# Kernel tuning notes

Hardware: AMD Instinct MI355X
Metric: run time of the kernel (lower is better)

Reference implementation:

```python
import jax, jax.numpy as jnp
import numpy as np

EXTENT = 1.0  # kernel-point influence radius (init kwarg 'extent')
B, N, M, H, K, F, C = 4, 16384, 16384, 32, 15, 64, 64


def setup_inputs() -> dict:
    key = jax.random.key(0)
    ks = jax.random.split(key, 6)
    points = jax.random.uniform(ks[0], (B, N, 3), dtype=jnp.float32)
    features = jax.random.normal(ks[1], (B, N, F), dtype=jnp.float32)
    output_points = jax.random.uniform(ks[2], (B, M, 3), dtype=jnp.float32)
    neighbor_indices = jax.random.randint(ks[3], (B, M, H), 0, N)
    # kernel point dispositions inside a ball of radius 1.5*extent (load_kernels stand-in)
    k_points = jax.random.uniform(ks[4], (K, 3), minval=-1.0, maxval=1.0, dtype=jnp.float32) * (1.5 * EXTENT) / jnp.sqrt(3.0)
    k_values = jax.random.normal(ks[5], (K, F, C), dtype=jnp.float32) * 0.05
    return {
        'points': points, 'features': features, 'output_points': output_points,
        'k_points': k_points, 'k_values': k_values, 'neighbor_indices': neighbor_indices,
    }


def reference(points, features, output_points, k_points, k_values, neighbor_indices):
    b, m, h = neighbor_indices.shape
    idx = neighbor_indices.reshape(b, m * h, 1)
    # batched gather (tf.gather batch_dims=1)
    neigh_pts = jnp.take_along_axis(points, idx, axis=1).reshape(b, m, h, 3)
    neigh_feat = jnp.take_along_axis(features, idx, axis=1).reshape(b, m, h, -1)
    # relative coords to each output point, then to each kernel point
    rel = neigh_pts - output_points[:, :, None, :]                # [B,M,H,3]
    diff = rel[:, :, :, None, :] - k_points                       # [B,M,H,K,3]
    sq_d = jnp.sum(diff * diff, axis=-1)                          # [B,M,H,K]
    # linear influence
    w = jnp.maximum(1.0 - jnp.sqrt(sq_d) / EXTENT, 0.0)           # [B,M,H,K]
    # weight neighbor features per kernel point, then apply per-kernel linear map, sum over K
    wf = jnp.einsum('bmhk,bmhf->bmkf', w, neigh_feat)             # [B,M,K,F]
    out = jnp.einsum('bmkf,kfc->bmc', wf, k_values)               # [B,M,C]
    return out
```

## Files before the change

kernel.cpp:

```cpp
#include <hip/hip_runtime.h>

#define BATCH 4
#define NPTS 16384
#define MPTS 16384
#define NH 32
#define NK 15
#define NF 64
#define NC 64
#define MT 16

typedef short short8 __attribute__((ext_vector_type(8)));
typedef float floatx4 __attribute__((ext_vector_type(4)));

__device__ __forceinline__ unsigned short f2bf(float x) {
    unsigned int u = __builtin_bit_cast(unsigned int, x);
    u = u + 0x7FFFu + ((u >> 16) & 1u);
    return (unsigned short)(u >> 16);
}

__device__ __forceinline__ unsigned pack_trunc(float lo, float hi) {
    return __builtin_amdgcn_perm(__builtin_bit_cast(unsigned, hi),
                                 __builtin_bit_cast(unsigned, lo), 0x07060302u);
}

__global__ void feat_cvt_kernel(const float* __restrict__ src, unsigned short* __restrict__ dst) {
    const int gid = blockIdx.x * 256 + threadIdx.x;
    const size_t base = (size_t)gid * 8;
    float4 a = *(const float4*)(src + base);
    float4 b = *(const float4*)(src + base + 4);
    uint4 o;
    o.x = (unsigned)f2bf(a.x) | ((unsigned)f2bf(a.y) << 16);
    o.y = (unsigned)f2bf(a.z) | ((unsigned)f2bf(a.w) << 16);
    o.z = (unsigned)f2bf(b.x) | ((unsigned)f2bf(b.y) << 16);
    o.w = (unsigned)f2bf(b.z) | ((unsigned)f2bf(b.w) << 16);
    *(uint4*)(dst + base) = o;
}

__global__ void vprep_kernel(const float* __restrict__ kv, unsigned short* __restrict__ vp) {
    const int gid = blockIdx.x * 256 + threadIdx.x;
    const int lane = gid & 63;
    const int ct   = (gid >> 6) & 3;
    const int kk   = gid >> 8;
    const int c    = ct * 16 + (lane & 15);
    const int kap0 = kk * 32 + (lane >> 4) * 8;
    unsigned int o[4];
    #pragma unroll
    for (int jj = 0; jj < 4; jj++) {
        unsigned short lo, hi;
        {
            const int kap = kap0 + jj * 2;
            const int f = kap >> 4, k = kap & 15;
            lo = (k < NK) ? f2bf(kv[((size_t)(k * NF + f)) * NC + c]) : (unsigned short)0;
        }
        {
            const int kap = kap0 + jj * 2 + 1;
            const int f = kap >> 4, k = kap & 15;
            hi = (k < NK) ? f2bf(kv[((size_t)(k * NF + f)) * NC + c]) : (unsigned short)0;
        }
        o[jj] = (unsigned)lo | ((unsigned)hi << 16);
    }
    *(uint4*)(vp + (size_t)gid * 8) = make_uint4(o[0], o[1], o[2], o[3]);
}

__global__ __launch_bounds__(256, 3) void kpconv_kernel(
    const float* __restrict__ points,
    const unsigned short* __restrict__ featbf,
    const float* __restrict__ outpts,
    const float* __restrict__ kpts,
    const unsigned short* __restrict__ vp,
    const int*   __restrict__ nbr,
    float* __restrict__ out)
{
    __shared__ unsigned short awf[32 * 512];
    __shared__ unsigned short feat_s[4 * 1288];
    __shared__ float4 rel_s[4 * 32];
    __shared__ int   idx_s[512];
    __shared__ float opt_s[48];
    __shared__ float kp_s[48];

    const int tid   = threadIdx.x;
    const int batch = blockIdx.x >> 10;
    const int m0    = (blockIdx.x & 1023) << 4;

    if (tid < 48) kp_s[tid] = (tid < 45) ? kpts[tid] : 1e9f;
    if (tid >= 64 && tid < 112)
        opt_s[tid - 64] = outpts[(size_t)(batch * MPTS + m0) * 3 + (tid - 64)];
    {
        const size_t nb = (size_t)(batch * MPTS + m0) * NH;
        idx_s[tid]       = nbr[nb + tid];
        idx_s[256 + tid] = nbr[nb + 256 + tid];
    }
    __syncthreads();

    const int g    = tid >> 6;
    const int lane = tid & 63;
    const int cl   = lane & 15;
    const int q    = lane >> 4;

    for (int r = 0; r < 4; r++) {
        const int spl = tid >> 6;
        const int sa  = tid & 15;
        const int sfc = (tid >> 4) & 3;
        const int srow = (r * 4 + spl) * 32 + sa * 2;
        const int id0 = idx_s[srow], id1 = idx_s[srow + 1];
        const unsigned short* s0p = featbf + ((size_t)(batch * NPTS) + id0) * NF + sfc * 8;
        const unsigned short* s1p = featbf + ((size_t)(batch * NPTS) + id1) * NF + sfc * 8;
        unsigned short* dp = &feat_s[spl * 1288 + (sfc * 8) * 40 + sa * 2];

        {
            uint4 ra = *(const uint4*)s0p;
            uint4 rb = *(const uint4*)s1p;
            *(unsigned*)(dp + 0 * 40) = __builtin_amdgcn_perm(rb.x, ra.x, 0x05040100u);
            *(unsigned*)(dp + 1 * 40) = __builtin_amdgcn_perm(rb.x, ra.x, 0x07060302u);
            *(unsigned*)(dp + 2 * 40) = __builtin_amdgcn_perm(rb.y, ra.y, 0x05040100u);
            *(unsigned*)(dp + 3 * 40) = __builtin_amdgcn_perm(rb.y, ra.y, 0x07060302u);
            *(unsigned*)(dp + 4 * 40) = __builtin_amdgcn_perm(rb.z, ra.z, 0x05040100u);
            *(unsigned*)(dp + 5 * 40) = __builtin_amdgcn_perm(rb.z, ra.z, 0x07060302u);
            *(unsigned*)(dp + 6 * 40) = __builtin_amdgcn_perm(rb.w, ra.w, 0x05040100u);
            *(unsigned*)(dp + 7 * 40) = __builtin_amdgcn_perm(rb.w, ra.w, 0x07060302u);
        }
        if (tid < 128) {
            const int rpl = tid >> 5, rh = tid & 31;
            const int rid = idx_s[(r * 4 + rpl) * 32 + rh];
            const float* pp = points + ((size_t)(batch * NPTS) + rid) * 3;
            const int p = r * 4 + rpl;
            rel_s[rpl * 32 + rh] = make_float4(pp[0] - opt_s[p * 3 + 0],
                                               pp[1] - opt_s[p * 3 + 1],
                                               pp[2] - opt_s[p * 3 + 2], 0.f);
        }
        __syncthreads();

        const int p = r * 4 + g;
        short8 af;
        {
            const float kx = kp_s[cl * 3 + 0];
            const float ky = kp_s[cl * 3 + 1];
            const float kz = kp_s[cl * 3 + 2];
            float wv[8];
            #pragma unroll
            for (int j = 0; j < 8; j++) {
                const float4 rr = rel_s[g * 32 + q * 8 + j];
                const float dx = rr.x - kx, dy = rr.y - ky, dz = rr.z - kz;
                const float d = sqrtf(dx * dx + dy * dy + dz * dz);
                wv[j] = fmaxf(1.f - d, 0.f);
            }
            uint4 ua;
            ua.x = pack_trunc(wv[0], wv[1]);
            ua.y = pack_trunc(wv[2], wv[3]);
            ua.z = pack_trunc(wv[4], wv[5]);
            ua.w = pack_trunc(wv[6], wv[7]);
            af = __builtin_bit_cast(short8, ua);
        }
        #pragma unroll
        for (int t = 0; t < 2; t++) {
            const uint4 ub = *(const uint4*)&feat_s[g * 1288 + (t * 16 + cl) * 40 + q * 8];
            floatx4 dd = {0.f, 0.f, 0.f, 0.f};
            dd = __builtin_amdgcn_mfma_f32_16x16x32_bf16(af, __builtin_bit_cast(short8, ub), dd, 0, 0, 0);
            const int kk    = 8 * t + (cl >> 1);
            const int q2    = (2 * cl + (q >> 1)) & 3;
            const int chunk = (p ^ (kk & 15)) | (q2 << 4);
            unsigned* wp = (unsigned*)awf + kk * 256 + chunk * 4 + (q & 1) * 2;
            wp[0] = pack_trunc(dd[0], dd[1]);
            wp[1] = pack_trunc(dd[2], dd[3]);
        }
        __syncthreads();

        {
            uint4 ra = *(const uint4*)(s0p + 32);
            uint4 rb = *(const uint4*)(s1p + 32);
            *(unsigned*)(dp + 0 * 40) = __builtin_amdgcn_perm(rb.x, ra.x, 0x05040100u);
            *(unsigned*)(dp + 1 * 40) = __builtin_amdgcn_perm(rb.x, ra.x, 0x07060302u);
            *(unsigned*)(dp + 2 * 40) = __builtin_amdgcn_perm(rb.y, ra.y, 0x05040100u);
            *(unsigned*)(dp + 3 * 40) = __builtin_amdgcn_perm(rb.y, ra.y, 0x07060302u);
            *(unsigned*)(dp + 4 * 40) = __builtin_amdgcn_perm(rb.z, ra.z, 0x05040100u);
            *(unsigned*)(dp + 5 * 40) = __builtin_amdgcn_perm(rb.z, ra.z, 0x07060302u);
            *(unsigned*)(dp + 6 * 40) = __builtin_amdgcn_perm(rb.w, ra.w, 0x05040100u);
            *(unsigned*)(dp + 7 * 40) = __builtin_amdgcn_perm(rb.w, ra.w, 0x07060302u);
        }
        __syncthreads();

        #pragma unroll
        for (int t = 2; t < 4; t++) {
            const uint4 ub = *(const uint4*)&feat_s[g * 1288 + ((t - 2) * 16 + cl) * 40 + q * 8];
            floatx4 dd = {0.f, 0.f, 0.f, 0.f};
            dd = __builtin_amdgcn_mfma_f32_16x16x32_bf16(af, __builtin_bit_cast(short8, ub), dd, 0, 0, 0);
            const int kk    = 8 * t + (cl >> 1);
            const int q2    = (2 * cl + (q >> 1)) & 3;
            const int chunk = (p ^ (kk & 15)) | (q2 << 4);
            unsigned* wp = (unsigned*)awf + kk * 256 + chunk * 4 + (q & 1) * 2;
            wp[0] = pack_trunc(dd[0], dd[1]);
            wp[1] = pack_trunc(dd[2], dd[3]);
        }
        __syncthreads();
    }

    floatx4 acc0 = {0.f, 0.f, 0.f, 0.f};
    floatx4 acc1 = {0.f, 0.f, 0.f, 0.f};
    const unsigned short* vpg = vp + g * 512 + lane * 8;
    #pragma unroll 8
    for (int kk = 0; kk < 32; kk++) {
        const int chunk = ((lane & 15) ^ (kk & 15)) | (lane & 48);
        const uint4 uA = *(const uint4*)&awf[kk * 512 + chunk * 8];
        const uint4 uB = *(const uint4*)(vpg + (size_t)kk * 2048);
        if (kk & 1)
            acc1 = __builtin_amdgcn_mfma_f32_16x16x32_bf16(
                __builtin_bit_cast(short8, uA), __builtin_bit_cast(short8, uB), acc1, 0, 0, 0);
        else
            acc0 = __builtin_amdgcn_mfma_f32_16x16x32_bf16(
                __builtin_bit_cast(short8, uA), __builtin_bit_cast(short8, uB), acc0, 0, 0, 0);
    }
    const floatx4 acc = acc0 + acc1;

    #pragma unroll
    for (int ri = 0; ri < 4; ri++) {
        out[((size_t)(batch * MPTS + m0 + q * 4 + ri)) * NC + g * 16 + cl] = acc[ri];
    }
}

extern "C" void kernel_launch(void* const* d_in, const int* in_sizes, int n_in,
                              void* d_out, int out_size, void* d_ws, size_t ws_size,
                              hipStream_t stream) {
    const float* points   = (const float*)d_in[0];
    const float* features = (const float*)d_in[1];
    const float* outpts   = (const float*)d_in[2];
    const float* kpts     = (const float*)d_in[3];
    const float* kvals    = (const float*)d_in[4];
    const int*   nbr      = (const int*)d_in[5];
    float* out = (float*)d_out;

    unsigned short* vp     = (unsigned short*)d_ws;
    unsigned short* featbf = (unsigned short*)((char*)d_ws + 131072);

    vprep_kernel<<<32, 256, 0, stream>>>(kvals, vp);
    feat_cvt_kernel<<<2048, 256, 0, stream>>>(features, featbf);

    const int blocks = BATCH * (MPTS / MT);
    kpconv_kernel<<<blocks, 256, 0, stream>>>(points, featbf, outpts, kpts, vp, nbr, out);
}
```

Before: 163.8 us.

## Restructure KPConv kernel with register-prefetched gathers, halved LDS, and fused prep

Merges the two preprocessing kernels into a single launch. In the main kernel, all kernel-point weights are computed up front into registers, and the relative coordinates reuse the awf buffer. The feature-half loop is reordered so the second-stage MFMA contraction runs in two halves of 16 k-steps, which halves the awf shared buffer and allows occupancy to rise from 3 to 5 blocks. The next neighbor feature gather is prefetched into registers while the current tile's MFMAs run, and intra-wave barriers are dropped between tiles. The cost is more live registers (af[4], prefetch buffers), which the higher launch-bounds target may squeeze.

Measured after the change: 143.5 us. 1.14x faster.

```diff
diff --git a/kernel.cpp b/kernel.cpp
--- a/kernel.cpp
+++ b/kernel.cpp
@@ -23,46 +23,47 @@
                                  __builtin_bit_cast(unsigned, lo), 0x07060302u);
 }
 
-__global__ void feat_cvt_kernel(const float* __restrict__ src, unsigned short* __restrict__ dst) {
-    const int gid = blockIdx.x * 256 + threadIdx.x;
-    const size_t base = (size_t)gid * 8;
-    float4 a = *(const float4*)(src + base);
-    float4 b = *(const float4*)(src + base + 4);
-    uint4 o;
-    o.x = (unsigned)f2bf(a.x) | ((unsigned)f2bf(a.y) << 16);
-    o.y = (unsigned)f2bf(a.z) | ((unsigned)f2bf(a.w) << 16);
-    o.z = (unsigned)f2bf(b.x) | ((unsigned)f2bf(b.y) << 16);
-    o.w = (unsigned)f2bf(b.z) | ((unsigned)f2bf(b.w) << 16);
-    *(uint4*)(dst + base) = o;
-}
-
-__global__ void vprep_kernel(const float* __restrict__ kv, unsigned short* __restrict__ vp) {
-    const int gid = blockIdx.x * 256 + threadIdx.x;
-    const int lane = gid & 63;
-    const int ct   = (gid >> 6) & 3;
-    const int kk   = gid >> 8;
-    const int c    = ct * 16 + (lane & 15);
-    const int kap0 = kk * 32 + (lane >> 4) * 8;
-    unsigned int o[4];
-    #pragma unroll
-    for (int jj = 0; jj < 4; jj++) {
-        unsigned short lo, hi;
-        {
-            const int kap = kap0 + jj * 2;
-            const int f = kap >> 4, k = kap & 15;
-            lo = (k < NK) ? f2bf(kv[((size_t)(k * NF + f)) * NC + c]) : (unsigned short)0;
-        }
-        {
-            const int kap = kap0 + jj * 2 + 1;
-            const int f = kap >> 4, k = kap & 15;
-            hi = (k < NK) ? f2bf(kv[((size_t)(k * NF + f)) * NC + c]) : (unsigned short)0;
-        }
-        o[jj] = (unsigned)lo | ((unsigned)hi << 16);
-    }
-    *(uint4*)(vp + (size_t)gid * 8) = make_uint4(o[0], o[1], o[2], o[3]);
-}
-
-__global__ __launch_bounds__(256, 3) void kpconv_kernel(
+__global__ void prep_kernel(const float* __restrict__ kv, const float* __restrict__ feat,
+                            unsigned short* __restrict__ vp, unsigned short* __restrict__ featbf) {
+    if (blockIdx.x < 32) {
+        const int gid = blockIdx.x * 256 + threadIdx.x;
+        const int lane = gid & 63;
+        const int ct   = (gid >> 6) & 3;
+        const int kk   = gid >> 8;
+        const int c    = ct * 16 + (lane & 15);
+        const int kap0 = kk * 32 + (lane >> 4) * 8;
+        unsigned int o[4];
+        #pragma unroll
+        for (int jj = 0; jj < 4; jj++) {
+            unsigned short lo, hi;
+            {
+                const int kap = kap0 + jj * 2;
+                const int f = kap >> 4, k = kap & 15;
+                lo = (k < NK) ? f2bf(kv[((size_t)(k * NF + f)) * NC + c]) : (unsigned short)0;
+            }
+            {
+                const int kap = kap0 + jj * 2 + 1;
+                const int f = kap >> 4, k = kap & 15;
+                hi = (k < NK) ? f2bf(kv[((size_t)(k * NF + f)) * NC + c]) : (unsigned short)0;
+            }
+            o[jj] = (unsigned)lo | ((unsigned)hi << 16);
+        }
+        *(uint4*)(vp + (size_t)gid * 8) = make_uint4(o[0], o[1], o[2], o[3]);
+    } else {
+        const int gid = (blockIdx.x - 32) * 256 + threadIdx.x;
+        const size_t base = (size_t)gid * 8;
+        float4 a = *(const float4*)(feat + base);
+        float4 b = *(const float4*)(feat + base + 4);
+        uint4 o;
+        o.x = (unsigned)f2bf(a.x) | ((unsigned)f2bf(a.y) << 16);
+        o.y = (unsigned)f2bf(a.z) | ((unsigned)f2bf(a.w) << 16);
+        o.z = (unsigned)f2bf(b.x) | ((unsigned)f2bf(b.y) << 16);
+        o.w = (unsigned)f2bf(b.z) | ((unsigned)f2bf(b.w) << 16);
+        *(uint4*)(featbf + base) = o;
+    }
+}
+
+__global__ __launch_bounds__(256, 5) void kpconv_kernel(
     const float* __restrict__ points,
     const unsigned short* __restrict__ featbf,
     const float* __restrict__ outpts,
@@ -71,9 +72,8 @@
     const int*   __restrict__ nbr,
     float* __restrict__ out)
 {
-    __shared__ unsigned short awf[32 * 512];
+    __shared__ __align__(16) unsigned short awf[16 * 512];
     __shared__ unsigned short feat_s[4 * 1288];
-    __shared__ float4 rel_s[4 * 32];
     __shared__ int   idx_s[512];
     __shared__ float opt_s[48];
     __shared__ float kp_s[48];
@@ -96,50 +96,44 @@
     const int lane = tid & 63;
     const int cl   = lane & 15;
     const int q    = lane >> 4;
-
-    for (int r = 0; r < 4; r++) {
-        const int spl = tid >> 6;
-        const int sa  = tid & 15;
-        const int sfc = (tid >> 4) & 3;
-        const int srow = (r * 4 + spl) * 32 + sa * 2;
+    const int sa   = cl;
+    const int sfc  = q;
+
+    const unsigned short* fbase = featbf + (size_t)(batch * NPTS) * NF;
+
+    uint4 pra, prb;
+    {
+        const int srow = g * 32 + sa * 2;
         const int id0 = idx_s[srow], id1 = idx_s[srow + 1];
-        const unsigned short* s0p = featbf + ((size_t)(batch * NPTS) + id0) * NF + sfc * 8;
-        const unsigned short* s1p = featbf + ((size_t)(batch * NPTS) + id1) * NF + sfc * 8;
-        unsigned short* dp = &feat_s[spl * 1288 + (sfc * 8) * 40 + sa * 2];
-
-        {
-            uint4 ra = *(const uint4*)s0p;
-            uint4 rb = *(const uint4*)s1p;
-            *(unsigned*)(dp + 0 * 40) = __builtin_amdgcn_perm(rb.x, ra.x, 0x05040100u);
-            *(unsigned*)(dp + 1 * 40) = __builtin_amdgcn_perm(rb.x, ra.x, 0x07060302u);
-            *(unsigned*)(dp + 2 * 40) = __builtin_amdgcn_perm(rb.y, ra.y, 0x05040100u);
-            *(unsigned*)(dp + 3 * 40) = __builtin_amdgcn_perm(rb.y, ra.y, 0x07060302u);
-            *(unsigned*)(dp + 4 * 40) = __builtin_amdgcn_perm(rb.z, ra.z, 0x05040100u);
-            *(unsigned*)(dp + 5 * 40) = __builtin_amdgcn_perm(rb.z, ra.z, 0x07060302u);
-            *(unsigned*)(dp + 6 * 40) = __builtin_amdgcn_perm(rb.w, ra.w, 0x05040100u);
-            *(unsigned*)(dp + 7 * 40) = __builtin_amdgcn_perm(rb.w, ra.w, 0x07060302u);
-        }
-        if (tid < 128) {
-            const int rpl = tid >> 5, rh = tid & 31;
-            const int rid = idx_s[(r * 4 + rpl) * 32 + rh];
-            const float* pp = points + ((size_t)(batch * NPTS) + rid) * 3;
-            const int p = r * 4 + rpl;
-            rel_s[rpl * 32 + rh] = make_float4(pp[0] - opt_s[p * 3 + 0],
-                                               pp[1] - opt_s[p * 3 + 1],
-                                               pp[2] - opt_s[p * 3 + 2], 0.f);
-        }
-        __syncthreads();
-
-        const int p = r * 4 + g;
-        short8 af;
-        {
-            const float kx = kp_s[cl * 3 + 0];
-            const float ky = kp_s[cl * 3 + 1];
-            const float kz = kp_s[cl * 3 + 2];
+        pra = *(const uint4*)(fbase + (size_t)id0 * NF + sfc * 8);
+        prb = *(const uint4*)(fbase + (size_t)id1 * NF + sfc * 8);
+    }
+
+    float4* rel4 = (float4*)awf;
+    #pragma unroll
+    for (int rr = 0; rr < 2; rr++) {
+        const int row = tid * 2 + rr;
+        const int id  = idx_s[row];
+        const int pm  = row >> 5;
+        const float* pp = points + ((size_t)(batch * NPTS) + id) * 3;
+        rel4[row] = make_float4(pp[0] - opt_s[pm * 3 + 0],
+                                pp[1] - opt_s[pm * 3 + 1],
+                                pp[2] - opt_s[pm * 3 + 2], 0.f);
+    }
+    __syncthreads();
+
+    short8 af[4];
+    {
+        const float kx = kp_s[cl * 3 + 0];
+        const float ky = kp_s[cl * 3 + 1];
+        const float kz = kp_s[cl * 3 + 2];
+        #pragma unroll
+        for (int rp = 0; rp < 4; rp++) {
+            const int p = rp * 4 + g;
             float wv[8];
             #pragma unroll
             for (int j = 0; j < 8; j++) {
-                const float4 rr = rel_s[g * 32 + q * 8 + j];
+                const float4 rr = rel4[p * 32 + q * 8 + j];
                 const float dx = rr.x - kx, dy = rr.y - ky, dz = rr.z - kz;
                 const float d = sqrtf(dx * dx + dy * dy + dz * dz);
                 wv[j] = fmaxf(1.f - d, 0.f);
@@ -149,59 +143,76 @@
             ua.y = pack_trunc(wv[2], wv[3]);
             ua.z = pack_trunc(wv[4], wv[5]);
             ua.w = pack_trunc(wv[6], wv[7]);
-            af = __builtin_bit_cast(short8, ua);
-        }
+            af[rp] = __builtin_bit_cast(short8, ua);
+        }
+    }
+    __syncthreads();
+
+    floatx4 acc0 = {0.f, 0.f, 0.f, 0.f};
+    floatx4 acc1 = {0.f, 0.f, 0.f, 0.f};
+    const unsigned short* vpg = vp + g * 512 + lane * 8;
+    unsigned short* dp = &feat_s[g * 1288 + (sfc * 8) * 40 + sa * 2];
+
+    #pragma unroll
+    for (int it = 0; it < 8; it++) {
+        const int r  = it & 3;
+        const int p  = r * 4 + g;
+
+        *(unsigned*)(dp + 0 * 40) = __builtin_amdgcn_perm(prb.x, pra.x, 0x05040100u);
+        *(unsigned*)(dp + 1 * 40) = __builtin_amdgcn_perm(prb.x, pra.x, 0x07060302u);
+        *(unsigned*)(dp + 2 * 40) = __builtin_amdgcn_perm(prb.y, pra.y, 0x05040100u);
+        *(unsigned*)(dp + 3 * 40) = __builtin_amdgcn_perm(prb.y, pra.y, 0x07060302u);
+        *(unsigned*)(dp + 4 * 40) = __builtin_amdgcn_perm(prb.z, pra.z, 0x05040100u);
+        *(unsigned*)(dp + 5 * 40) = __builtin_amdgcn_perm(prb.z, pra.z, 0x07060302u);
+        *(unsigned*)(dp + 6 * 40) = __builtin_amdgcn_perm(prb.w, pra.w, 0x05040100u);
+        *(unsigned*)(dp + 7 * 40) = __builtin_amdgcn_perm(prb.w, pra.w, 0x07060302u);
+
+        if (it < 7) {
+            const int nit = it + 1;
+            const int nfh = nit >> 2, nr = nit & 3;
+            const int srow = (nr * 4 + g) * 32 + sa * 2;
+            const int id0 = idx_s[srow], id1 = idx_s[srow + 1];
+            pra = *(const uint4*)(fbase + (size_t)id0 * NF + nfh * 32 + sfc * 8);
+            prb = *(const uint4*)(fbase + (size_t)id1 * NF + nfh * 32 + sfc * 8);
+        }
+
         #pragma unroll
         for (int t = 0; t < 2; t++) {
             const uint4 ub = *(const uint4*)&feat_s[g * 1288 + (t * 16 + cl) * 40 + q * 8];
             floatx4 dd = {0.f, 0.f, 0.f, 0.f};
-            dd = __builtin_amdgcn_mfma_f32_16x16x32_bf16(af, __builtin_bit_cast(short8, ub), dd, 0, 0, 0);
+            dd = __builtin_amdgcn_mfma_f32_16x16x32_bf16(af[r], __builtin_bit_cast(short8, ub), dd, 0, 0, 0);
             const int kk    = 8 * t + (cl >> 1);
             const int q2    = (2 * cl + (q >> 1)) & 3;
-            const int chunk = (p ^ (kk & 15)) | (q2 << 4);
+            const int chunk = (p ^ kk) | (q2 << 4);
             unsigned* wp = (unsigned*)awf + kk * 256 + chunk * 4 + (q & 1) * 2;
             wp[0] = pack_trunc(dd[0], dd[1]);
             wp[1] = pack_trunc(dd[2], dd[3]);
         }
-        __syncthreads();
-
-        {
-            uint4 ra = *(const uint4*)(s0p + 32);
-            uint4 rb = *(const uint4*)(s1p + 32);
-            *(unsigned*)(dp + 0 * 40) = __builtin_amdgcn_perm(rb.x, ra.x, 0x05040100u);
-            *(unsigned*)(dp + 1 * 40) = __builtin_amdgcn_perm(rb.x, ra.x, 0x07060302u);
-            *(unsigned*)(dp + 2 * 40) = __builtin_amdgcn_perm(rb.y, ra.y, 0x05040100u);
-            *(unsigned*)(dp + 3 * 40) = __builtin_amdgcn_perm(rb.y, ra.y, 0x07060302u);
-            *(unsigned*)(dp + 4 * 40) = __builtin_amdgcn_perm(rb.z, ra.z, 0x05040100u);
-            *(unsigned*)(dp + 5 * 40) = __builtin_amdgcn_perm(rb.z, ra.z, 0x07060302u);
-            *(unsigned*)(dp + 6 * 40) = __builtin_amdgcn_perm(rb.w, ra.w, 0x05040100u);
-            *(unsigned*)(dp + 7 * 40) = __builtin_amdgcn_perm(rb.w, ra.w, 0x07060302u);
-        }
-        __syncthreads();
-
-        #pragma unroll
-        for (int t = 2; t < 4; t++) {
-            const uint4 ub = *(const uint4*)&feat_s[g * 1288 + ((t - 2) * 16 + cl) * 40 + q * 8];
-            floatx4 dd = {0.f, 0.f, 0.f, 0.f};
-            dd = __builtin_amdgcn_mfma_f32_16x16x32_bf16(af, __builtin_bit_cast(short8, ub), dd, 0, 0, 0);
-            const int kk    = 8 * t + (cl >> 1);
-            const int q2    = (2 * cl + (q >> 1)) & 3;
-            const int chunk = (p ^ (kk & 15)) | (q2 << 4);
-            unsigned* wp = (unsigned*)awf + kk * 256 + chunk * 4 + (q & 1) * 2;
-            wp[0] = pack_trunc(dd[0], dd[1]);
-            wp[1] = pack_trunc(dd[2], dd[3]);
-        }
-        __syncthreads();
-    }
-
-    floatx4 acc0 = {0.f, 0.f, 0.f, 0.f};
-    floatx4 acc1 = {0.f, 0.f, 0.f, 0.f};
-    const unsigned short* vpg = vp + g * 512 + lane * 8;
-    #pragma unroll 8
-    for (int kk = 0; kk < 32; kk++) {
-        const int chunk = ((lane & 15) ^ (kk & 15)) | (lane & 48);
+
+        if (it == 3) {
+            __syncthreads();
+            #pragma unroll 4
+            for (int kk = 0; kk < 16; kk++) {
+                const int chunk = (cl ^ kk) | (lane & 48);
+                const uint4 uA = *(const uint4*)&awf[kk * 512 + chunk * 8];
+                const uint4 uB = *(const uint4*)(vpg + (size_t)kk * 2048);
+                if (kk & 1)
+                    acc1 = __builtin_amdgcn_mfma_f32_16x16x32_bf16(
+                        __builtin_bit_cast(short8, uA), __builtin_bit_cast(short8, uB), acc1, 0, 0, 0);
+                else
+                    acc0 = __builtin_amdgcn_mfma_f32_16x16x32_bf16(
+                        __builtin_bit_cast(short8, uA), __builtin_bit_cast(short8, uB), acc0, 0, 0, 0);
+            }
+            __syncthreads();
+        }
+    }
+
+    __syncthreads();
+    #pragma unroll 4
+    for (int kk = 0; kk < 16; kk++) {
+        const int chunk = (cl ^ kk) | (lane & 48);
         const uint4 uA = *(const uint4*)&awf[kk * 512 + chunk * 8];
-        const uint4 uB = *(const uint4*)(vpg + (size_t)kk * 2048);
+        const uint4 uB = *(const uint4*)(vpg + (size_t)(16 + kk) * 2048);
         if (kk & 1)
             acc1 = __builtin_amdgcn_mfma_f32_16x16x32_bf16(
                 __builtin_bit_cast(short8, uA), __builtin_bit_cast(short8, uB), acc1, 0, 0, 0);
@@ -231,8 +242,7 @@
     unsigned short* vp     = (unsigned short*)d_ws;
     unsigned short* featbf = (unsigned short*)((char*)d_ws + 131072);
 
-    vprep_kernel<<<32, 256, 0, stream>>>(kvals, vp);
-    feat_cvt_kernel<<<2048, 256, 0, stream>>>(features, featbf);
+    prep_kernel<<<2080, 256, 0, stream>>>(kvals, features, vp, featbf);
 
     const int blocks = BATCH * (MPTS / MT);
     kpconv_kernel<<<blocks, 256, 0, stream>>>(points, featbf, outpts, kpts, vp, nbr, out);
```
